# Performance work log

Hardware: AMD Instinct MI355X
Metric: run time of the kernel (lower is better)

The kernel has to match this reference:

```python
import jax, jax.numpy as jnp
import numpy as np

N, D = 20000, 16          # nodes, fixed in-degree
IN, HID, OUT = 128, 128, 1


def _lstm_final_h(x_seq, Wih, Whh, bih, bhh):
    # x_seq: [D, N, F]; LSTM with hidden size H == F, zero init state.
    # Returns final hidden state h_D: [N, H]. PyTorch gate order i,f,g,o.
    Nn = x_seq.shape[1]
    H = Whh.shape[1]
    b = bih + bhh

    def step(carry, xt):
        h, c = carry
        gates = xt @ Wih.T + h @ Whh.T + b          # [N, 4H]
        i, f, g, o = jnp.split(gates, 4, axis=-1)
        c = jax.nn.sigmoid(f) * c + jax.nn.sigmoid(i) * jnp.tanh(g)
        h = jax.nn.sigmoid(o) * jnp.tanh(c)
        return (h, c), None

    init = (jnp.zeros((Nn, H), x_seq.dtype), jnp.zeros((Nn, H), x_seq.dtype))
    (h, _), _ = jax.lax.scan(step, init, x_seq)
    return h


def _sage_lstm(x, nbr_idx, Wih, Whh, bih, bhh, Wself, Wneigh, bneigh):
    # DGL SAGEConv(aggregator='lstm'): out = fc_self(x) + fc_neigh(lstm(neighbors))
    msgs = x[nbr_idx]                                # gather: [N, D, F]
    hN = _lstm_final_h(jnp.swapaxes(msgs, 0, 1), Wih, Whh, bih, bhh)  # [N, F]
    return x @ Wself.T + hN @ Wneigh.T + bneigh


def setup_inputs() -> dict:
    key = jax.random.key(0)
    ks = jax.random.split(key, 16)
    s = 1.0 / float(np.sqrt(IN))
    u = lambda k, sh: jax.random.uniform(k, sh, jnp.float32, -s, s)
    return {
        "x": jax.random.normal(ks[0], (N, IN), jnp.float32),
        "nbr_idx": jax.random.randint(ks[1], (N, D), 0, N),
        "Wih1": u(ks[2], (4 * IN, IN)), "Whh1": u(ks[3], (4 * IN, IN)),
        "bih1": u(ks[4], (4 * IN,)), "bhh1": u(ks[5], (4 * IN,)),
        "Wself1": u(ks[6], (HID, IN)), "Wneigh1": u(ks[7], (HID, IN)),
        "bneigh1": jnp.zeros((HID,), jnp.float32),
        "Wih2": u(ks[8], (4 * HID, HID)), "Whh2": u(ks[9], (4 * HID, HID)),
        "bih2": u(ks[10], (4 * HID,)), "bhh2": u(ks[11], (4 * HID,)),
        "Wself2": u(ks[12], (OUT, HID)), "Wneigh2": u(ks[13], (OUT, HID)),
        "bneigh2": jnp.zeros((OUT,), jnp.float32),
    }


def reference(x, nbr_idx, Wih1, Whh1, bih1, bhh1, Wself1, Wneigh1, bneigh1,
              Wih2, Whh2, bih2, bhh2, Wself2, Wneigh2, bneigh2):
    h = _sage_lstm(x, nbr_idx, Wih1, Whh1, bih1, bhh1, Wself1, Wneigh1, bneigh1)
    h = jax.nn.relu(h)
    h = _sage_lstm(h, nbr_idx, Wih2, Whh2, bih2, bhh2, Wself2, Wneigh2, bneigh2)
    return jax.nn.sigmoid(h)
```

## Files before the change

### kernel.cpp

```cpp
#include <hip/hip_runtime.h>


#define NN   20000
#define L2E  1.4426950408889634f

typedef unsigned short u16;
typedef __attribute__((ext_vector_type(8))) short frag8;
typedef __attribute__((ext_vector_type(4))) float facc4;
typedef __attribute__((ext_vector_type(8))) _Float16 half8;

#define OFF_X16   0u
#define OFF_H1    5120000u
#define OFF_HN    10240000u
#define OFF_WIH1P 15360000u
#define OFF_WHH1P 15491072u
#define OFF_WIH2P 15622144u
#define OFF_WHH2P 15753216u
#define OFF_WS1P  15884288u
#define OFF_WN1P  15917056u
#define OFF_WS2B  15949824u
#define OFF_WN2B  15950080u
#define OFF_B1    15950336u
#define OFF_B2    15952384u
#define OFF_XPRE  15954432u

__device__ __forceinline__ u16 f2bf(float f) {
  union { float f; unsigned u; } v; v.f = f;
  unsigned r = (v.u + 0x7fffu + ((v.u >> 16) & 1u)) >> 16;
  return (u16)r;
}
__device__ __forceinline__ float bflo(unsigned u) {
  union { unsigned u; float f; } v; v.u = u << 16; return v.f;
}
__device__ __forceinline__ float bfhi(unsigned u) {
  union { unsigned u; float f; } v; v.u = u & 0xffff0000u; return v.f;
}
__device__ __forceinline__ unsigned pk2h(float a, float b) {
  union { _Float16 h[2]; unsigned u; } v;
  v.h[0] = (_Float16)a; v.h[1] = (_Float16)b;
  return v.u;
}
__device__ __forceinline__ unsigned pkbf(float a, float b) {
  unsigned r;
  asm("v_cvt_pk_bf16_f32 %0, %1, %2" : "=v"(r) : "v"(a), "v"(b));
  return r;
}
__device__ __forceinline__ facc4 mfma16(frag8 a, frag8 b, facc4 c) {
  return __builtin_amdgcn_mfma_f32_16x16x32_bf16(a, b, c, 0, 0, 0);
}
__device__ __forceinline__ float sigm_ps(float xp) {
  return __builtin_amdgcn_rcpf(1.f + __builtin_amdgcn_exp2f(-xp));
}
__device__ __forceinline__ float tanh_ps(float xp) {
  return 1.f - 2.f * __builtin_amdgcn_rcpf(1.f + __builtin_amdgcn_exp2f(xp));
}
__device__ __forceinline__ float gate_scale(int row) {
  return (row >= 256 && row < 384) ? 2.f * L2E : L2E;
}

__device__ __forceinline__ void pack512(u16* dst, const float* src, int i) {
  int e = i & 7, ln = (i >> 3) & 63, kb = (i >> 9) & 3, tj = i >> 11;
  int row = tj * 16 + (ln & 15);
  int col = kb * 32 + (ln >> 4) * 8 + e;
  dst[i] = f2bf(src[row * 128 + col] * gate_scale(row));
}
__device__ __forceinline__ void pack128(u16* dst, const float* src, int i) {
  int e = i & 7, ln = (i >> 3) & 63, kb = (i >> 9) & 3, tj = i >> 11;
  dst[i] = f2bf(src[(tj * 16 + (ln & 15)) * 128 + kb * 32 + (ln >> 4) * 8 + e]);
}

__global__ __launch_bounds__(256) void pack_kernel(
    const float* __restrict__ x,
    const float* __restrict__ Wih1, const float* __restrict__ Whh1,
    const float* __restrict__ bih1, const float* __restrict__ bhh1,
    const float* __restrict__ Wself1, const float* __restrict__ Wneigh1,
    const float* __restrict__ Wih2, const float* __restrict__ Whh2,
    const float* __restrict__ bih2, const float* __restrict__ bhh2,
    const float* __restrict__ Wself2, const float* __restrict__ Wneigh2,
    char* __restrict__ ws)
{
  int i = blockIdx.x * 256 + threadIdx.x;
  if (i < 2560000) { ((u16*)(ws + OFF_X16))[i] = f2bf(x[i]); return; }
  i -= 2560000;
  if (i < 65536) { pack512((u16*)(ws + OFF_WIH1P), Wih1, i); return; }
  i -= 65536;
  if (i < 65536) { pack512((u16*)(ws + OFF_WHH1P), Whh1, i); return; }
  i -= 65536;
  if (i < 65536) { pack512((u16*)(ws + OFF_WIH2P), Wih2, i); return; }
  i -= 65536;
  if (i < 65536) { pack512((u16*)(ws + OFF_WHH2P), Whh2, i); return; }
  i -= 65536;
  if (i < 16384) { pack128((u16*)(ws + OFF_WS1P), Wself1, i); return; }
  i -= 16384;
  if (i < 16384) { pack128((u16*)(ws + OFF_WN1P), Wneigh1, i); return; }
  i -= 16384;
  if (i < 128) { ((u16*)(ws + OFF_WS2B))[i] = f2bf(Wself2[i]); return; }
  i -= 128;
  if (i < 128) { ((u16*)(ws + OFF_WN2B))[i] = f2bf(Wneigh2[i]); return; }
  i -= 128;
  if (i < 512) { ((float*)(ws + OFF_B1))[i] = (bih1[i] + bhh1[i]) * gate_scale(i); return; }
  i -= 512;
  if (i < 512) { ((float*)(ws + OFF_B2))[i] = (bih2[i] + bhh2[i]) * gate_scale(i); }
}

__global__ __launch_bounds__(256) void xpre_kernel(
    const u16* __restrict__ inp,
    const frag8* __restrict__ Wp,
    const float* __restrict__ bias,
    u16* __restrict__ outp)
{
  __shared__ __align__(16) u16 stage[64][512];
  const int tid = threadIdx.x;
  const int lane = tid & 63, wave = tid >> 6;
  const int m = lane & 15, quad = lane >> 4;
  const int row = blockIdx.x * 64 + wave * 16 + m;
  if (row < NN) {
    frag8 bfr[4];
#pragma unroll
    for (int kb = 0; kb < 4; ++kb)
      bfr[kb] = *(const frag8*)(inp + (size_t)row * 128 + kb * 32 + quad * 8);
    u16* srow = stage[wave * 16 + m];
#pragma unroll
    for (int tj = 0; tj < 32; ++tj) {
      float4 bv = *(const float4*)(bias + tj * 16 + quad * 4);
      facc4 acc = {bv.x, bv.y, bv.z, bv.w};
#pragma unroll
      for (int kb = 0; kb < 4; ++kb)
        acc = mfma16(Wp[(tj * 4 + kb) * 64 + lane], bfr[kb], acc);
      uint2 st = { pk2h(acc[0], acc[1]), pk2h(acc[2], acc[3]) };
      *(uint2*)(srow + (tj & 7) * 64 + quad * 16 + (tj >> 3) * 4) = st;
    }
  }
  __syncthreads();
  const int base = blockIdx.x * 64;
#pragma unroll
  for (int i = tid; i < 4096; i += 256) {
    int r = i >> 6, cc = i & 63;
    int n = base + r;
    if (n < NN)
      ((uint4*)(outp + (size_t)n * 512))[cc] = ((const uint4*)stage[r])[cc];
  }
}

__global__ __launch_bounds__(512, 4) void lstm_kernel(
    const u16* __restrict__ Xpre,
    const frag8* __restrict__ Wp,
    const int* __restrict__ nbr,
    u16* __restrict__ hN)
{
  __shared__ __align__(16) u16 h_lds[2][16 * 136];
  const int tid = threadIdx.x;
  const int lane = tid & 63, g = tid >> 6;
  const int m = lane & 15, quad = lane >> 4;

  frag8 A[4][4];
#pragma unroll
  for (int gate = 0; gate < 4; ++gate)
#pragma unroll
    for (int kb = 0; kb < 4; ++kb)
      A[gate][kb] = Wp[((gate * 8 + g) * 4 + kb) * 64 + lane];

  for (int i = tid; i < 16 * 136; i += 512) h_lds[0][i] = 0;

  const int node_base = blockIdx.x * 16;
  int4 idx4 = *(const int4*)(nbr + (size_t)(node_base + m) * 16 + quad * 4);

  facc4 c = {0.f, 0.f, 0.f, 0.f};

  auto xslice = [&](int t) -> const uint4* {
    const int tq = t >> 2, ts = t & 3;
    int sel = (ts == 0) ? idx4.x : (ts == 1) ? idx4.y : (ts == 2) ? idx4.z : idx4.w;
    int idx = __shfl(sel, m + (tq << 4), 64);
    return (const uint4*)(Xpre + (size_t)idx * 512) + g * 8 + quad * 2;
  };

  uint4 pX0, pX1;
  { const uint4* p0 = xslice(0); pX0 = p0[0]; pX1 = p0[1]; }

  __syncthreads();

#pragma unroll 1
  for (int t = 0; t < 16; ++t) {
    const u16* hr = h_lds[t & 1];
    u16* hw = h_lds[(t + 1) & 1];
    const uint4* pn = xslice(t < 15 ? t + 1 : 15);

    frag8 bfr[4];
#pragma unroll
    for (int kb = 0; kb < 4; ++kb)
      bfr[kb] = *(const frag8*)(hr + m * 136 + kb * 32 + quad * 8);

    union { uint4 u; half8 h; } ua, ub;
    ua.u = pX0; ub.u = pX1;
    facc4 ai = {(float)ua.h[0], (float)ua.h[1], (float)ua.h[2], (float)ua.h[3]};
    facc4 af = {(float)ua.h[4], (float)ua.h[5], (float)ua.h[6], (float)ua.h[7]};
    facc4 ag = {(float)ub.h[0], (float)ub.h[1], (float)ub.h[2], (float)ub.h[3]};
    facc4 ao = {(float)ub.h[4], (float)ub.h[5], (float)ub.h[6], (float)ub.h[7]};
    pX0 = pn[0]; pX1 = pn[1];

#pragma unroll
    for (int kb = 0; kb < 4; ++kb) {
      ai = mfma16(A[0][kb], bfr[kb], ai);
      af = mfma16(A[1][kb], bfr[kb], af);
      ag = mfma16(A[2][kb], bfr[kb], ag);
      ao = mfma16(A[3][kb], bfr[kb], ao);
    }

    facc4 hv;
#pragma unroll
    for (int r = 0; r < 4; ++r) {
      float si = sigm_ps(ai[r]);
      float sf = sigm_ps(af[r]);
      float tg = tanh_ps(ag[r]);
      float cn = sf * c[r] + si * tg;
      c[r] = cn;
      float so = sigm_ps(ao[r]);
      hv[r] = so * tanh_ps((2.f * L2E) * cn);
    }
    uint2 hp = { pkbf(hv[0], hv[1]), pkbf(hv[2], hv[3]) };

    if (t < 15) {
      *(uint2*)(hw + m * 136 + g * 16 + quad * 4) = hp;
      asm volatile("s_waitcnt lgkmcnt(0)" ::: "memory");
      __builtin_amdgcn_s_barrier();
    } else {
      *(uint2*)(hN + (size_t)(node_base + m) * 128 + g * 16 + quad * 4) = hp;
    }
  }
}

__global__ __launch_bounds__(256) void out1_kernel(
    const u16* __restrict__ x16, const u16* __restrict__ hN,
    const frag8* __restrict__ Wsp, const frag8* __restrict__ Wnp,
    const float* __restrict__ bneigh, u16* __restrict__ h1)
{
  __shared__ __align__(16) u16 stage[64][128];
  const int tid = threadIdx.x;
  const int lane = tid & 63, wave = tid >> 6;
  const int m = lane & 15, quad = lane >> 4;
  const int row = blockIdx.x * 64 + wave * 16 + m;
  if (row < NN) {
    frag8 bx[4], bh[4];
#pragma unroll
    for (int kb = 0; kb < 4; ++kb) {
      bx[kb] = *(const frag8*)(x16 + (size_t)row * 128 + kb * 32 + quad * 8);
      bh[kb] = *(const frag8*)(hN + (size_t)row * 128 + kb * 32 + quad * 8);
    }
    u16* srow = stage[wave * 16 + m];
#pragma unroll
    for (int tj = 0; tj < 8; ++tj) {
      float4 bv = *(const float4*)(bneigh + tj * 16 + quad * 4);
      facc4 acc = {bv.x, bv.y, bv.z, bv.w};
#pragma unroll
      for (int kb = 0; kb < 4; ++kb) {
        acc = mfma16(Wsp[(tj * 4 + kb) * 64 + lane], bx[kb], acc);
        acc = mfma16(Wnp[(tj * 4 + kb) * 64 + lane], bh[kb], acc);
      }
      uint2 st = { pkbf(fmaxf(acc[0], 0.f), fmaxf(acc[1], 0.f)),
                   pkbf(fmaxf(acc[2], 0.f), fmaxf(acc[3], 0.f)) };
      *(uint2*)(srow + tj * 16 + quad * 4) = st;
    }
  }
  __syncthreads();
  const int base = blockIdx.x * 64;
#pragma unroll
  for (int i = tid; i < 1024; i += 256) {
    int r = i >> 4, cc = i & 15;
    int n = base + r;
    if (n < NN)
      ((uint4*)(h1 + (size_t)n * 128))[cc] = ((const uint4*)stage[r])[cc];
  }
}

__device__ __forceinline__ float dot2(unsigned a, unsigned b) {
  return bflo(a) * bflo(b) + bfhi(a) * bfhi(b);
}

__global__ __launch_bounds__(256) void out2_kernel(
    const u16* __restrict__ h1, const u16* __restrict__ hN2,
    const u16* __restrict__ ws2, const u16* __restrict__ wn2,
    const float* __restrict__ b2, float* __restrict__ outp)
{
  int n = blockIdx.x * 256 + threadIdx.x;
  if (n >= NN) return;
  const uint4* r1 = (const uint4*)(h1 + (size_t)n * 128);
  const uint4* r2 = (const uint4*)(hN2 + (size_t)n * 128);
  const uint4* w1 = (const uint4*)ws2;
  const uint4* w2 = (const uint4*)wn2;
  float acc = b2[0];
#pragma unroll
  for (int q = 0; q < 16; ++q) {
    uint4 a = r1[q], w = w1[q];
    acc += dot2(a.x, w.x) + dot2(a.y, w.y) + dot2(a.z, w.z) + dot2(a.w, w.w);
    uint4 c = r2[q], v = w2[q];
    acc += dot2(c.x, v.x) + dot2(c.y, v.y) + dot2(c.z, v.z) + dot2(c.w, v.w);
  }
  outp[n] = __builtin_amdgcn_rcpf(1.f + __builtin_amdgcn_exp2f(-acc * L2E));
}

extern "C" void kernel_launch(void* const* d_in, const int* in_sizes, int n_in,
                              void* d_out, int out_size, void* d_ws, size_t ws_size,
                              hipStream_t stream) {
  const float* x       = (const float*)d_in[0];
  const int*   nbr     = (const int*)d_in[1];
  const float* Wih1    = (const float*)d_in[2];
  const float* Whh1    = (const float*)d_in[3];
  const float* bih1    = (const float*)d_in[4];
  const float* bhh1    = (const float*)d_in[5];
  const float* Wself1  = (const float*)d_in[6];
  const float* Wneigh1 = (const float*)d_in[7];
  const float* bneigh1 = (const float*)d_in[8];
  const float* Wih2    = (const float*)d_in[9];
  const float* Whh2    = (const float*)d_in[10];
  const float* bih2    = (const float*)d_in[11];
  const float* bhh2    = (const float*)d_in[12];
  const float* Wself2  = (const float*)d_in[13];
  const float* Wneigh2 = (const float*)d_in[14];
  const float* bneigh2 = (const float*)d_in[15];

  char* ws = (char*)d_ws;
  u16*   x16   = (u16*)(ws + OFF_X16);
  u16*   h1    = (u16*)(ws + OFF_H1);
  u16*   hN    = (u16*)(ws + OFF_HN);
  u16*   Xpre  = (u16*)(ws + OFF_XPRE);
  frag8* Wih1p = (frag8*)(ws + OFF_WIH1P);
  frag8* Whh1p = (frag8*)(ws + OFF_WHH1P);
  frag8* Wih2p = (frag8*)(ws + OFF_WIH2P);
  frag8* Whh2p = (frag8*)(ws + OFF_WHH2P);
  frag8* Ws1p  = (frag8*)(ws + OFF_WS1P);
  frag8* Wn1p  = (frag8*)(ws + OFF_WN1P);
  u16*   Ws2b  = (u16*)(ws + OFF_WS2B);
  u16*   Wn2b  = (u16*)(ws + OFF_WN2B);
  float* b1    = (float*)(ws + OFF_B1);
  float* b2    = (float*)(ws + OFF_B2);

  pack_kernel<<<11157, 256, 0, stream>>>(x, Wih1, Whh1, bih1, bhh1, Wself1,
                                         Wneigh1, Wih2, Whh2, bih2, bhh2,
                                         Wself2, Wneigh2, ws);
  xpre_kernel<<<313, 256, 0, stream>>>(x16, Wih1p, b1, Xpre);
  lstm_kernel<<<1250, 512, 0, stream>>>(Xpre, Whh1p, nbr, hN);
  out1_kernel<<<313, 256, 0, stream>>>(x16, hN, Ws1p, Wn1p, bneigh1, h1);
  xpre_kernel<<<313, 256, 0, stream>>>(h1, Wih2p, b2, Xpre);
  lstm_kernel<<<1250, 512, 0, stream>>>(Xpre, Whh2p, nbr, hN);
  out2_kernel<<<79, 256, 0, stream>>>(h1, hN, Ws2b, Wn2b, bneigh2, (float*)d_out);
}
```

Baseline: 263.6 us.

## Fuse output projections into LSTM kernel epilogue and widen xpre/pack kernels

The layer-1 output projection (self+neighbor matmul with ReLU) and the layer-2 final dot-product plus sigmoid now run as an epilogue of the LSTM kernel. They read the final hidden state straight from LDS, so the hN round trip through global memory and two kernel launches go away. The xpre kernel moves to 512 threads, with each wave doing half the gate tiles, and the pack kernel converts x four elements per thread. The epilogue runs on the LSTM's 16-node blocks, which adds a little per-block work and one extra barrier.

```diff
diff --git a/kernel.cpp b/kernel.cpp
--- a/kernel.cpp
+++ b/kernel.cpp
@@ -11,7 +11,6 @@
 
 #define OFF_X16   0u
 #define OFF_H1    5120000u
-#define OFF_HN    10240000u
 #define OFF_WIH1P 15360000u
 #define OFF_WHH1P 15491072u
 #define OFF_WIH2P 15622144u
@@ -57,6 +56,9 @@
 __device__ __forceinline__ float gate_scale(int row) {
   return (row >= 256 && row < 384) ? 2.f * L2E : L2E;
 }
+__device__ __forceinline__ float dot2(unsigned a, unsigned b) {
+  return bflo(a) * bflo(b) + bfhi(a) * bfhi(b);
+}
 
 __device__ __forceinline__ void pack512(u16* dst, const float* src, int i) {
   int e = i & 7, ln = (i >> 3) & 63, kb = (i >> 9) & 3, tj = i >> 11;
@@ -80,8 +82,13 @@
     char* __restrict__ ws)
 {
   int i = blockIdx.x * 256 + threadIdx.x;
-  if (i < 2560000) { ((u16*)(ws + OFF_X16))[i] = f2bf(x[i]); return; }
-  i -= 2560000;
+  if (i < 640000) {
+    float4 v = ((const float4*)x)[i];
+    uint2 st = { pkbf(v.x, v.y), pkbf(v.z, v.w) };
+    ((uint2*)(ws + OFF_X16))[i] = st;
+    return;
+  }
+  i -= 640000;
   if (i < 65536) { pack512((u16*)(ws + OFF_WIH1P), Wih1, i); return; }
   i -= 65536;
   if (i < 65536) { pack512((u16*)(ws + OFF_WHH1P), Whh1, i); return; }
@@ -103,7 +110,7 @@
   if (i < 512) { ((float*)(ws + OFF_B2))[i] = (bih2[i] + bhh2[i]) * gate_scale(i); }
 }
 
-__global__ __launch_bounds__(256) void xpre_kernel(
+__global__ __launch_bounds__(512) void xpre_kernel(
     const u16* __restrict__ inp,
     const frag8* __restrict__ Wp,
     const float* __restrict__ bias,
@@ -113,15 +120,17 @@
   const int tid = threadIdx.x;
   const int lane = tid & 63, wave = tid >> 6;
   const int m = lane & 15, quad = lane >> 4;
-  const int row = blockIdx.x * 64 + wave * 16 + m;
+  const int rg = wave & 3, jh = wave >> 2;
+  const int row = blockIdx.x * 64 + rg * 16 + m;
   if (row < NN) {
     frag8 bfr[4];
 #pragma unroll
     for (int kb = 0; kb < 4; ++kb)
       bfr[kb] = *(const frag8*)(inp + (size_t)row * 128 + kb * 32 + quad * 8);
-    u16* srow = stage[wave * 16 + m];
-#pragma unroll
-    for (int tj = 0; tj < 32; ++tj) {
+    u16* srow = stage[rg * 16 + m];
+#pragma unroll
+    for (int j = 0; j < 16; ++j) {
+      const int tj = jh * 16 + j;
       float4 bv = *(const float4*)(bias + tj * 16 + quad * 4);
       facc4 acc = {bv.x, bv.y, bv.z, bv.w};
 #pragma unroll
@@ -134,7 +143,7 @@
   __syncthreads();
   const int base = blockIdx.x * 64;
 #pragma unroll
-  for (int i = tid; i < 4096; i += 256) {
+  for (int i = tid; i < 4096; i += 512) {
     int r = i >> 6, cc = i & 63;
     int n = base + r;
     if (n < NN)
@@ -146,7 +155,14 @@
     const u16* __restrict__ Xpre,
     const frag8* __restrict__ Wp,
     const int* __restrict__ nbr,
-    u16* __restrict__ hN)
+    const u16* __restrict__ xin,
+    const frag8* __restrict__ Wsp, const frag8* __restrict__ Wnp,
+    const float* __restrict__ bias_o,
+    const u16* __restrict__ ws2, const u16* __restrict__ wn2,
+    const float* __restrict__ b2,
+    u16* __restrict__ h1,
+    float* __restrict__ outp,
+    int mode)
 {
   __shared__ __align__(16) u16 h_lds[2][16 * 136];
   const int tid = threadIdx.x;
@@ -218,84 +234,53 @@
       hv[r] = so * tanh_ps((2.f * L2E) * cn);
     }
     uint2 hp = { pkbf(hv[0], hv[1]), pkbf(hv[2], hv[3]) };
-
-    if (t < 15) {
-      *(uint2*)(hw + m * 136 + g * 16 + quad * 4) = hp;
-      asm volatile("s_waitcnt lgkmcnt(0)" ::: "memory");
-      __builtin_amdgcn_s_barrier();
-    } else {
-      *(uint2*)(hN + (size_t)(node_base + m) * 128 + g * 16 + quad * 4) = hp;
-    }
-  }
-}
-
-__global__ __launch_bounds__(256) void out1_kernel(
-    const u16* __restrict__ x16, const u16* __restrict__ hN,
-    const frag8* __restrict__ Wsp, const frag8* __restrict__ Wnp,
-    const float* __restrict__ bneigh, u16* __restrict__ h1)
-{
-  __shared__ __align__(16) u16 stage[64][128];
-  const int tid = threadIdx.x;
-  const int lane = tid & 63, wave = tid >> 6;
-  const int m = lane & 15, quad = lane >> 4;
-  const int row = blockIdx.x * 64 + wave * 16 + m;
-  if (row < NN) {
+    *(uint2*)(hw + m * 136 + g * 16 + quad * 4) = hp;
+    asm volatile("s_waitcnt lgkmcnt(0)" ::: "memory");
+    __builtin_amdgcn_s_barrier();
+  }
+
+  const u16* hf = h_lds[0];
+
+  if (mode == 0) {
+    const int row = node_base + m;
     frag8 bx[4], bh[4];
 #pragma unroll
     for (int kb = 0; kb < 4; ++kb) {
-      bx[kb] = *(const frag8*)(x16 + (size_t)row * 128 + kb * 32 + quad * 8);
-      bh[kb] = *(const frag8*)(hN + (size_t)row * 128 + kb * 32 + quad * 8);
-    }
-    u16* srow = stage[wave * 16 + m];
-#pragma unroll
-    for (int tj = 0; tj < 8; ++tj) {
-      float4 bv = *(const float4*)(bneigh + tj * 16 + quad * 4);
-      facc4 acc = {bv.x, bv.y, bv.z, bv.w};
-#pragma unroll
-      for (int kb = 0; kb < 4; ++kb) {
-        acc = mfma16(Wsp[(tj * 4 + kb) * 64 + lane], bx[kb], acc);
-        acc = mfma16(Wnp[(tj * 4 + kb) * 64 + lane], bh[kb], acc);
-      }
-      uint2 st = { pkbf(fmaxf(acc[0], 0.f), fmaxf(acc[1], 0.f)),
-                   pkbf(fmaxf(acc[2], 0.f), fmaxf(acc[3], 0.f)) };
-      *(uint2*)(srow + tj * 16 + quad * 4) = st;
-    }
-  }
-  __syncthreads();
-  const int base = blockIdx.x * 64;
-#pragma unroll
-  for (int i = tid; i < 1024; i += 256) {
-    int r = i >> 4, cc = i & 15;
-    int n = base + r;
-    if (n < NN)
-      ((uint4*)(h1 + (size_t)n * 128))[cc] = ((const uint4*)stage[r])[cc];
-  }
-}
-
-__device__ __forceinline__ float dot2(unsigned a, unsigned b) {
-  return bflo(a) * bflo(b) + bfhi(a) * bfhi(b);
-}
-
-__global__ __launch_bounds__(256) void out2_kernel(
-    const u16* __restrict__ h1, const u16* __restrict__ hN2,
-    const u16* __restrict__ ws2, const u16* __restrict__ wn2,
-    const float* __restrict__ b2, float* __restrict__ outp)
-{
-  int n = blockIdx.x * 256 + threadIdx.x;
-  if (n >= NN) return;
-  const uint4* r1 = (const uint4*)(h1 + (size_t)n * 128);
-  const uint4* r2 = (const uint4*)(hN2 + (size_t)n * 128);
-  const uint4* w1 = (const uint4*)ws2;
-  const uint4* w2 = (const uint4*)wn2;
-  float acc = b2[0];
-#pragma unroll
-  for (int q = 0; q < 16; ++q) {
-    uint4 a = r1[q], w = w1[q];
-    acc += dot2(a.x, w.x) + dot2(a.y, w.y) + dot2(a.z, w.z) + dot2(a.w, w.w);
-    uint4 c = r2[q], v = w2[q];
-    acc += dot2(c.x, v.x) + dot2(c.y, v.y) + dot2(c.z, v.z) + dot2(c.w, v.w);
-  }
-  outp[n] = __builtin_amdgcn_rcpf(1.f + __builtin_amdgcn_exp2f(-acc * L2E));
+      bx[kb] = *(const frag8*)(xin + (size_t)row * 128 + kb * 32 + quad * 8);
+      bh[kb] = *(const frag8*)(hf + m * 136 + kb * 32 + quad * 8);
+    }
+    float4 bv = *(const float4*)(bias_o + g * 16 + quad * 4);
+    facc4 acc = {bv.x, bv.y, bv.z, bv.w};
+#pragma unroll
+    for (int kb = 0; kb < 4; ++kb) {
+      frag8 wsk = Wsp[(g * 4 + kb) * 64 + lane];
+      acc = mfma16(wsk, bx[kb], acc);
+      frag8 wnk = Wnp[(g * 4 + kb) * 64 + lane];
+      acc = mfma16(wnk, bh[kb], acc);
+    }
+    uint2 st = { pkbf(fmaxf(acc[0], 0.f), fmaxf(acc[1], 0.f)),
+                 pkbf(fmaxf(acc[2], 0.f), fmaxf(acc[3], 0.f)) };
+    u16* stg = (u16*)h_lds[1];
+    *(uint2*)(stg + m * 136 + g * 16 + quad * 4) = st;
+    __syncthreads();
+    const int r = tid >> 5, cc = tid & 31;
+    *(uint2*)(h1 + (size_t)(node_base + r) * 128 + cc * 4) =
+        *(const uint2*)(stg + r * 136 + cc * 4);
+  } else {
+    const int n = tid >> 5, cc = tid & 31;
+    uint2 a = *(const uint2*)(h1 + (size_t)(node_base + n) * 128 + cc * 4);
+    uint2 w = *(const uint2*)(ws2 + cc * 4);
+    uint2 b = *(const uint2*)(hf + n * 136 + cc * 4);
+    uint2 v = *(const uint2*)(wn2 + cc * 4);
+    float p = dot2(a.x, w.x) + dot2(a.y, w.y) + dot2(b.x, v.x) + dot2(b.y, v.y);
+#pragma unroll
+    for (int s = 1; s < 32; s <<= 1) p += __shfl_xor(p, s, 64);
+    if (cc == 0) {
+      float acc = p + b2[0];
+      outp[node_base + n] =
+          __builtin_amdgcn_rcpf(1.f + __builtin_amdgcn_exp2f(-acc * L2E));
+    }
+  }
 }
 
 extern "C" void kernel_launch(void* const* d_in, const int* in_sizes, int n_in,
@@ -321,7 +306,6 @@
   char* ws = (char*)d_ws;
   u16*   x16   = (u16*)(ws + OFF_X16);
   u16*   h1    = (u16*)(ws + OFF_H1);
-  u16*   hN    = (u16*)(ws + OFF_HN);
   u16*   Xpre  = (u16*)(ws + OFF_XPRE);
   frag8* Wih1p = (frag8*)(ws + OFF_WIH1P);
   frag8* Whh1p = (frag8*)(ws + OFF_WHH1P);
@@ -334,13 +318,15 @@
   float* b1    = (float*)(ws + OFF_B1);
   float* b2    = (float*)(ws + OFF_B2);
 
-  pack_kernel<<<11157, 256, 0, stream>>>(x, Wih1, Whh1, bih1, bhh1, Wself1,
-                                         Wneigh1, Wih2, Whh2, bih2, bhh2,
-                                         Wself2, Wneigh2, ws);
-  xpre_kernel<<<313, 256, 0, stream>>>(x16, Wih1p, b1, Xpre);
-  lstm_kernel<<<1250, 512, 0, stream>>>(Xpre, Whh1p, nbr, hN);
-  out1_kernel<<<313, 256, 0, stream>>>(x16, hN, Ws1p, Wn1p, bneigh1, h1);
-  xpre_kernel<<<313, 256, 0, stream>>>(h1, Wih2p, b2, Xpre);
-  lstm_kernel<<<1250, 512, 0, stream>>>(Xpre, Whh2p, nbr, hN);
-  out2_kernel<<<79, 256, 0, stream>>>(h1, hN, Ws2b, Wn2b, bneigh2, (float*)d_out);
-}
+  pack_kernel<<<3657, 256, 0, stream>>>(x, Wih1, Whh1, bih1, bhh1, Wself1,
+                                        Wneigh1, Wih2, Whh2, bih2, bhh2,
+                                        Wself2, Wneigh2, ws);
+  xpre_kernel<<<313, 512, 0, stream>>>(x16, Wih1p, b1, Xpre);
+  lstm_kernel<<<1250, 512, 0, stream>>>(Xpre, Whh1p, nbr, x16, Ws1p, Wn1p,
+                                        bneigh1, Ws2b, Wn2b, bneigh2, h1,
+                                        (float*)d_out, 0);
+  xpre_kernel<<<313, 512, 0, stream>>>(h1, Wih2p, b2, Xpre);
+  lstm_kernel<<<1250, 512, 0, stream>>>(Xpre, Whh2p, nbr, x16, Ws1p, Wn1p,
+                                        bneigh1, Ws2b, Wn2b, bneigh2, h1,
+                                        (float*)d_out, 1);
+}
```

Measured after the change: 258.2 us. -2.0%, faster.
